# Kernel optimization log

Measured on AMD Instinct MI355X. Metric: run time of the kernel, lower is better.

Reference implementation:

```python
import jax, jax.numpy as jnp
import numpy as np

HEAD_SIZE = 64
HEADS = 12

def _rope(x):
    # x: [B, L, d]; bert4torch interleaved RoPE: q*cos + rotate_every_two(q)*sin
    L, d = x.shape[-2], x.shape[-1]
    inv_freq = 1.0 / (10000.0 ** (jnp.arange(0, d, 2, dtype=jnp.float32) / d))
    ang = jnp.arange(L, dtype=jnp.float32)[:, None] * inv_freq  # [L, d/2]
    sin = jnp.repeat(jnp.sin(ang), 2, axis=-1)  # [L, d]
    cos = jnp.repeat(jnp.cos(ang), 2, axis=-1)  # [L, d]
    x2 = jnp.stack([-x[..., 1::2], x[..., ::2]], axis=-1).reshape(x.shape)
    return x * cos + x2 * sin

def setup_inputs() -> dict:
    key = jax.random.key(0)
    ks = jax.random.split(key, 4)
    B, L, H = 2, 2048, 1024
    inputs = jax.random.normal(ks[0], (B, L, H), dtype=jnp.float32)
    mask = jnp.ones((B, L), dtype=jnp.int32)
    Wp = jax.random.normal(ks[1], (H, 2 * HEAD_SIZE), dtype=jnp.float32) * (1.0 / np.sqrt(H))
    bp = jnp.zeros((2 * HEAD_SIZE,), dtype=jnp.float32)
    Wq = jax.random.normal(ks[2], (2 * HEAD_SIZE, 2 * HEADS), dtype=jnp.float32) * (1.0 / np.sqrt(2 * HEAD_SIZE))
    bq = jnp.zeros((2 * HEADS,), dtype=jnp.float32)
    return {"inputs": inputs, "mask": mask, "Wp": Wp, "bp": bp, "Wq": Wq, "bq": bq}

def reference(inputs, mask, Wp, bp, Wq, bq):
    B, L, _ = inputs.shape
    seq_out = inputs @ Wp + bp                          # [B, L, 2*hs]
    qw, kw = seq_out[..., :HEAD_SIZE], seq_out[..., HEAD_SIZE:]
    qw, kw = _rope(qw), _rope(kw)
    scores = jnp.einsum('bmd,bnd->bmn', qw, kw) / jnp.sqrt(jnp.float32(HEAD_SIZE))  # [B, L, L]
    # chunk(heads, -1) + stack(-2) == reshape(B, L, heads, 2); transpose(1,2) -> [B, H, L, 2]
    bias = (seq_out @ Wq + bq).reshape(B, L, HEADS, 2) / 2.0
    bias = jnp.transpose(bias, (0, 2, 1, 3))            # [B, H, L, 2]
    logits = scores[:, None] + bias[..., :1] + jnp.swapaxes(bias[..., 1:], 2, 3)  # [B, H, L, L]
    m = mask.astype(bool)
    neg_inf = jnp.float32(-jnp.inf)
    logits = jnp.where(m[:, None, :, None], logits, neg_inf)
    logits = jnp.where(m[:, None, None, :], logits, neg_inf)
    tril = jnp.tril(jnp.ones((L, L), dtype=logits.dtype), -1)
    logits = logits - tril * jnp.float32(1e12)
    return logits
```

## Files before the change

### kernel.cpp

```cpp
#include <hip/hip_runtime.h>
#include <math.h>

#define LSEQ 2048
#define NB 2
#define HDIM 1024
#define NKV 128
#define MALL (NB*LSEQ)
#define KSPLIT 4

__global__ __launch_bounds__(256) void k1_gemm(const float* __restrict__ A,
                                               const float* __restrict__ Wp,
                                               float* __restrict__ Cp) {
    const int nt    = blockIdx.x & 1;
    const int split = blockIdx.x >> 1;
    const int m0 = blockIdx.y * 64;
    const int n0 = nt * 64;
    __shared__ float As[32][68];
    __shared__ float Bs[32][64];
    const int tid = threadIdx.x;
    const int tm = tid & 15;
    const int tn = tid >> 4;
    float acc[4][4] = {};
    for (int kc = 0; kc < 8; ++kc) {
        const int k0 = split*256 + kc*32;
        #pragma unroll
        for (int p = 0; p < 2; ++p) {
            int idx = tid + 256*p;
            int row = idx >> 3, kq = idx & 7;
            float4 a = *(const float4*)(A + (size_t)(m0+row)*HDIM + k0 + 4*kq);
            As[4*kq+0][row] = a.x;
            As[4*kq+1][row] = a.y;
            As[4*kq+2][row] = a.z;
            As[4*kq+3][row] = a.w;
        }
        #pragma unroll
        for (int p = 0; p < 2; ++p) {
            int idx = tid + 256*p;
            int r = idx >> 4, c = idx & 15;
            *(float4*)(&Bs[r][4*c]) = *(const float4*)(Wp + (size_t)(k0+r)*NKV + n0 + 4*c);
        }
        __syncthreads();
        #pragma unroll
        for (int kk = 0; kk < 32; ++kk) {
            float4 av = *(const float4*)(&As[kk][4*tm]);
            float4 bv = *(const float4*)(&Bs[kk][4*tn]);
            float aa[4] = {av.x, av.y, av.z, av.w};
            float bb[4] = {bv.x, bv.y, bv.z, bv.w};
            #pragma unroll
            for (int i = 0; i < 4; ++i)
                #pragma unroll
                for (int j = 0; j < 4; ++j)
                    acc[i][j] = fmaf(aa[i], bb[j], acc[i][j]);
        }
        __syncthreads();
    }
    float* outp = Cp + (size_t)split*MALL*NKV;
    #pragma unroll
    for (int i = 0; i < 4; ++i) {
        float4 v = make_float4(acc[i][0], acc[i][1], acc[i][2], acc[i][3]);
        *(float4*)(outp + (size_t)(m0 + 4*tm + i)*NKV + n0 + 4*tn) = v;
    }
}

__global__ __launch_bounds__(64) void k2_rope_bias(const float* __restrict__ Cp,
        const float* __restrict__ bp, const float* __restrict__ Wq,
        const float* __restrict__ bq, float* __restrict__ qwout,
        float* __restrict__ kwout, float* __restrict__ biasQ,
        float* __restrict__ biasK) {
    const int row = blockIdx.x;
    const int b = row >> 11;
    const int l = row & (LSEQ - 1);
    const int t = threadIdx.x;
    float x0 = bp[2*t], x1 = bp[2*t+1];
    #pragma unroll
    for (int s = 0; s < KSPLIT; ++s) {
        const float* r = Cp + (size_t)s*MALL*NKV + (size_t)row*NKV;
        x0 += r[2*t];
        x1 += r[2*t+1];
    }
    const int p = t & 31;
    float inv = exp2f(-0.41524101186098287f * (float)p);
    float ang = (float)l * inv;
    float sn = sinf(ang), cs = cosf(ang);
    float y0 = x0*cs - x1*sn;
    float y1 = x1*cs + x0*sn;
    float* dst = (t < 32) ? (qwout + (size_t)row*64) : (kwout + (size_t)row*64);
    dst[2*p]   = y0;
    dst[2*p+1] = y1;
    float res = 0.f;
    for (int j = 0; j < 24; ++j) {
        float part = fmaf(x0, Wq[(2*t)*24 + j], x1 * Wq[(2*t+1)*24 + j]);
        #pragma unroll
        for (int off = 32; off > 0; off >>= 1)
            part += __shfl_xor(part, off);
        if (t == j) res = part;
    }
    if (t < 24) {
        float v = (res + bq[t]) * 0.5f;
        int h = t >> 1;
        float* bb = (t & 1) ? biasK : biasQ;
        bb[((size_t)b*12 + h)*LSEQ + l] = v;
    }
}

__global__ __launch_bounds__(256, 2) void k3_scores(const float* __restrict__ qw,
        const float* __restrict__ kwv, const float* __restrict__ biasQ,
        const float* __restrict__ biasK, const int* __restrict__ mask,
        float* __restrict__ out) {
    const int m0 = blockIdx.x * 4;
    const int b  = blockIdx.y;
    const int tid = threadIdx.x;
    const int nl = tid & 127;
    const int g  = tid >> 7;
    __shared__ float kws[128 * 68];

    const size_t rowbase = (size_t)b * LSEQ;
    const int mA = m0 + 2*g, mB = mA + 1;

    float4 q0[16], q1[16];
    {
        const float4* qp0 = (const float4*)(qw + (rowbase + mA)*64);
        const float4* qp1 = (const float4*)(qw + (rowbase + mB)*64);
        #pragma unroll
        for (int j = 0; j < 16; ++j) { q0[j] = qp0[j]; q1[j] = qp1[j]; }
    }
    float bq0[12], bq1[12];
    #pragma unroll
    for (int h = 0; h < 12; ++h) {
        const float* bqp = biasQ + ((size_t)b*12 + h)*LSEQ;
        bq0[h] = bqp[mA];
        bq1[h] = bqp[mB];
    }
    const bool okmA = mask[rowbase + mA] != 0;
    const bool okmB = mask[rowbase + mB] != 0;
    const size_t outbase = (size_t)b * 12 * LSEQ * LSEQ;

    for (int c = 0; c < 16; ++c) {
        const int nbase = c * 128;
        __syncthreads();
        #pragma unroll
        for (int p = 0; p < 8; ++p) {
            int f4 = tid + 256*p;
            int r = f4 >> 4, q16 = f4 & 15;
            float4 v = *(const float4*)(kwv + (rowbase + nbase + r)*64 + 4*q16);
            *(float4*)(&kws[r*68 + 4*q16]) = v;
        }
        __syncthreads();

        const int n = nbase + nl;
        float acc0 = 0.f, acc1 = 0.f;
        const float4* kr = (const float4*)(&kws[nl * 68]);
        #pragma unroll
        for (int j = 0; j < 16; ++j) {
            float4 kv = kr[j];
            acc0 = fmaf(q0[j].x, kv.x, acc0);
            acc0 = fmaf(q0[j].y, kv.y, acc0);
            acc0 = fmaf(q0[j].z, kv.z, acc0);
            acc0 = fmaf(q0[j].w, kv.w, acc0);
            acc1 = fmaf(q1[j].x, kv.x, acc1);
            acc1 = fmaf(q1[j].y, kv.y, acc1);
            acc1 = fmaf(q1[j].z, kv.z, acc1);
            acc1 = fmaf(q1[j].w, kv.w, acc1);
        }
        acc0 *= 0.125f;
        acc1 *= 0.125f;

        const bool okn = mask[rowbase + n] != 0;
        const float penA = (mA > n) ? 1e12f : 0.f;
        const float penB = (mB > n) ? 1e12f : 0.f;
        const bool okA = okmA && okn;
        const bool okB = okmB && okn;
        size_t offA = outbase + (size_t)mA * LSEQ + n;
        const float* bkp = biasK + (size_t)b*12*LSEQ + n;
        #pragma unroll
        for (int h = 0; h < 12; ++h) {
            float bk = bkp[(size_t)h * LSEQ];
            float v0 = acc0 + bq0[h] + bk;
            v0 = okA ? v0 : -INFINITY;
            v0 -= penA;
            float v1 = acc1 + bq1[h] + bk;
            v1 = okB ? v1 : -INFINITY;
            v1 -= penB;
            __builtin_nontemporal_store(v0, &out[offA + (size_t)h*LSEQ*LSEQ]);
            __builtin_nontemporal_store(v1, &out[offA + LSEQ + (size_t)h*LSEQ*LSEQ]);
        }
    }
}

extern "C" void kernel_launch(void* const* d_in, const int* in_sizes, int n_in,
                              void* d_out, int out_size, void* d_ws, size_t ws_size,
                              hipStream_t stream) {
    const float* inputs = (const float*)d_in[0];
    const int*   mask   = (const int*)  d_in[1];
    const float* Wp     = (const float*)d_in[2];
    const float* bp     = (const float*)d_in[3];
    const float* Wq     = (const float*)d_in[4];
    const float* bq     = (const float*)d_in[5];
    float* out = (float*)d_out;

    float* Cp  = (float*)d_ws;
    float* qwb = Cp  + (size_t)KSPLIT*MALL*NKV;
    float* kwb = qwb + (size_t)MALL*64;
    float* bQ  = kwb + (size_t)MALL*64;
    float* bK  = bQ  + (size_t)NB*12*LSEQ;

    k1_gemm     <<<dim3(8, 64),   256, 0, stream>>>(inputs, Wp, Cp);
    k2_rope_bias<<<dim3(MALL),     64, 0, stream>>>(Cp, bp, Wq, bq, qwb, kwb, bQ, bK);
    k3_scores   <<<dim3(512, 2), 256, 0, stream>>>(qwb, kwb, bQ, bK, mask, out);
}
```

Measured before the change: 465.9 us.

## Vectorize score stores, widen K tiles with swizzled LDS, retile projection GEMM

Measured after the change: 894.8 us. +92.1%, slower.

```diff
diff --git a/kernel.cpp b/kernel.cpp
--- a/kernel.cpp
+++ b/kernel.cpp
@@ -6,23 +6,23 @@
 #define HDIM 1024
 #define NKV 128
 #define MALL (NB*LSEQ)
-#define KSPLIT 4
+#define KSPLIT 8
+
+typedef float v4f __attribute__((ext_vector_type(4)));
 
 __global__ __launch_bounds__(256) void k1_gemm(const float* __restrict__ A,
                                                const float* __restrict__ Wp,
                                                float* __restrict__ Cp) {
-    const int nt    = blockIdx.x & 1;
-    const int split = blockIdx.x >> 1;
+    const int split = blockIdx.x;
     const int m0 = blockIdx.y * 64;
-    const int n0 = nt * 64;
     __shared__ float As[32][68];
-    __shared__ float Bs[32][64];
+    __shared__ float Bs[32][128];
     const int tid = threadIdx.x;
     const int tm = tid & 15;
     const int tn = tid >> 4;
-    float acc[4][4] = {};
-    for (int kc = 0; kc < 8; ++kc) {
-        const int k0 = split*256 + kc*32;
+    float acc[4][8] = {};
+    for (int kc = 0; kc < 4; ++kc) {
+        const int k0 = split*128 + kc*32;
         #pragma unroll
         for (int p = 0; p < 2; ++p) {
             int idx = tid + 256*p;
@@ -34,22 +34,23 @@
             As[4*kq+3][row] = a.w;
         }
         #pragma unroll
-        for (int p = 0; p < 2; ++p) {
+        for (int p = 0; p < 4; ++p) {
             int idx = tid + 256*p;
-            int r = idx >> 4, c = idx & 15;
-            *(float4*)(&Bs[r][4*c]) = *(const float4*)(Wp + (size_t)(k0+r)*NKV + n0 + 4*c);
+            int r = idx >> 5, c = idx & 31;
+            *(float4*)(&Bs[r][4*c]) = *(const float4*)(Wp + (size_t)(k0+r)*NKV + 4*c);
         }
         __syncthreads();
         #pragma unroll
         for (int kk = 0; kk < 32; ++kk) {
-            float4 av = *(const float4*)(&As[kk][4*tm]);
-            float4 bv = *(const float4*)(&Bs[kk][4*tn]);
+            float4 av  = *(const float4*)(&As[kk][4*tm]);
+            float4 bv0 = *(const float4*)(&Bs[kk][8*tn]);
+            float4 bv1 = *(const float4*)(&Bs[kk][8*tn+4]);
             float aa[4] = {av.x, av.y, av.z, av.w};
-            float bb[4] = {bv.x, bv.y, bv.z, bv.w};
+            float bb[8] = {bv0.x, bv0.y, bv0.z, bv0.w, bv1.x, bv1.y, bv1.z, bv1.w};
             #pragma unroll
             for (int i = 0; i < 4; ++i)
                 #pragma unroll
-                for (int j = 0; j < 4; ++j)
+                for (int j = 0; j < 8; ++j)
                     acc[i][j] = fmaf(aa[i], bb[j], acc[i][j]);
         }
         __syncthreads();
@@ -57,8 +58,9 @@
     float* outp = Cp + (size_t)split*MALL*NKV;
     #pragma unroll
     for (int i = 0; i < 4; ++i) {
-        float4 v = make_float4(acc[i][0], acc[i][1], acc[i][2], acc[i][3]);
-        *(float4*)(outp + (size_t)(m0 + 4*tm + i)*NKV + n0 + 4*tn) = v;
+        float* rp = outp + (size_t)(m0 + 4*tm + i)*NKV + 8*tn;
+        *(float4*)(rp)     = make_float4(acc[i][0], acc[i][1], acc[i][2], acc[i][3]);
+        *(float4*)(rp + 4) = make_float4(acc[i][4], acc[i][5], acc[i][6], acc[i][7]);
     }
 }
 
@@ -74,9 +76,9 @@
     float x0 = bp[2*t], x1 = bp[2*t+1];
     #pragma unroll
     for (int s = 0; s < KSPLIT; ++s) {
-        const float* r = Cp + (size_t)s*MALL*NKV + (size_t)row*NKV;
-        x0 += r[2*t];
-        x1 += r[2*t+1];
+        const float2 v = *(const float2*)(Cp + ((size_t)s*MALL + row)*NKV + 2*t);
+        x0 += v.x;
+        x1 += v.y;
     }
     const int p = t & 31;
     float inv = exp2f(-0.41524101186098287f * (float)p);
@@ -107,15 +109,15 @@
         const float* __restrict__ kwv, const float* __restrict__ biasQ,
         const float* __restrict__ biasK, const int* __restrict__ mask,
         float* __restrict__ out) {
-    const int m0 = blockIdx.x * 4;
+    const int m0 = blockIdx.x * 8;
     const int b  = blockIdx.y;
     const int tid = threadIdx.x;
-    const int nl = tid & 127;
-    const int g  = tid >> 7;
-    __shared__ float kws[128 * 68];
+    const int l   = tid & 63;
+    const int w   = tid >> 6;
+    __shared__ float4 kws4[4096];
 
     const size_t rowbase = (size_t)b * LSEQ;
-    const int mA = m0 + 2*g, mB = mA + 1;
+    const int mA = m0 + 2*w, mB = mA + 1;
 
     float4 q0[16], q1[16];
     {
@@ -134,55 +136,76 @@
     const bool okmA = mask[rowbase + mA] != 0;
     const bool okmB = mask[rowbase + mB] != 0;
     const size_t outbase = (size_t)b * 12 * LSEQ * LSEQ;
-
-    for (int c = 0; c < 16; ++c) {
-        const int nbase = c * 128;
-        __syncthreads();
-        #pragma unroll
-        for (int p = 0; p < 8; ++p) {
-            int f4 = tid + 256*p;
-            int r = f4 >> 4, q16 = f4 & 15;
-            float4 v = *(const float4*)(kwv + (rowbase + nbase + r)*64 + 4*q16);
-            *(float4*)(&kws[r*68 + 4*q16]) = v;
-        }
-        __syncthreads();
-
-        const int n = nbase + nl;
-        float acc0 = 0.f, acc1 = 0.f;
-        const float4* kr = (const float4*)(&kws[nl * 68]);
+    const float4* kg = (const float4*)(kwv + rowbase*64);
+
+    for (int c = 0; c < 8; ++c) {
+        const int nb = c * 256;
+        __syncthreads();
+        #pragma unroll 4
+        for (int p = 0; p < 16; ++p) {
+            int f4id = tid + 256*p;
+            int r = f4id >> 4, q = f4id & 15;
+            float4 v = kg[(size_t)(nb + r)*16 + q];
+            kws4[r*16 + ((q + (r >> 2)) & 15)] = v;
+        }
+        __syncthreads();
+
+        float accA[4] = {}, accB[4] = {};
         #pragma unroll
         for (int j = 0; j < 16; ++j) {
-            float4 kv = kr[j];
-            acc0 = fmaf(q0[j].x, kv.x, acc0);
-            acc0 = fmaf(q0[j].y, kv.y, acc0);
-            acc0 = fmaf(q0[j].z, kv.z, acc0);
-            acc0 = fmaf(q0[j].w, kv.w, acc0);
-            acc1 = fmaf(q1[j].x, kv.x, acc1);
-            acc1 = fmaf(q1[j].y, kv.y, acc1);
-            acc1 = fmaf(q1[j].z, kv.z, acc1);
-            acc1 = fmaf(q1[j].w, kv.w, acc1);
-        }
-        acc0 *= 0.125f;
-        acc1 *= 0.125f;
-
-        const bool okn = mask[rowbase + n] != 0;
-        const float penA = (mA > n) ? 1e12f : 0.f;
-        const float penB = (mB > n) ? 1e12f : 0.f;
-        const bool okA = okmA && okn;
-        const bool okB = okmB && okn;
-        size_t offA = outbase + (size_t)mA * LSEQ + n;
-        const float* bkp = biasK + (size_t)b*12*LSEQ + n;
+            const int rot = (j + l) & 15;
+            float4 k0v = kws4[(4*l + 0)*16 + rot];
+            float4 k1v = kws4[(4*l + 1)*16 + rot];
+            float4 k2v = kws4[(4*l + 2)*16 + rot];
+            float4 k3v = kws4[(4*l + 3)*16 + rot];
+            float4 qa = q0[j], qb = q1[j];
+            accA[0] = fmaf(qa.x, k0v.x, accA[0]); accA[0] = fmaf(qa.y, k0v.y, accA[0]);
+            accA[0] = fmaf(qa.z, k0v.z, accA[0]); accA[0] = fmaf(qa.w, k0v.w, accA[0]);
+            accA[1] = fmaf(qa.x, k1v.x, accA[1]); accA[1] = fmaf(qa.y, k1v.y, accA[1]);
+            accA[1] = fmaf(qa.z, k1v.z, accA[1]); accA[1] = fmaf(qa.w, k1v.w, accA[1]);
+            accA[2] = fmaf(qa.x, k2v.x, accA[2]); accA[2] = fmaf(qa.y, k2v.y, accA[2]);
+            accA[2] = fmaf(qa.z, k2v.z, accA[2]); accA[2] = fmaf(qa.w, k2v.w, accA[2]);
+            accA[3] = fmaf(qa.x, k3v.x, accA[3]); accA[3] = fmaf(qa.y, k3v.y, accA[3]);
+            accA[3] = fmaf(qa.z, k3v.z, accA[3]); accA[3] = fmaf(qa.w, k3v.w, accA[3]);
+            accB[0] = fmaf(qb.x, k0v.x, accB[0]); accB[0] = fmaf(qb.y, k0v.y, accB[0]);
+            accB[0] = fmaf(qb.z, k0v.z, accB[0]); accB[0] = fmaf(qb.w, k0v.w, accB[0]);
+            accB[1] = fmaf(qb.x, k1v.x, accB[1]); accB[1] = fmaf(qb.y, k1v.y, accB[1]);
+            accB[1] = fmaf(qb.z, k1v.z, accB[1]); accB[1] = fmaf(qb.w, k1v.w, accB[1]);
+            accB[2] = fmaf(qb.x, k2v.x, accB[2]); accB[2] = fmaf(qb.y, k2v.y, accB[2]);
+            accB[2] = fmaf(qb.z, k2v.z, accB[2]); accB[2] = fmaf(qb.w, k2v.w, accB[2]);
+            accB[3] = fmaf(qb.x, k3v.x, accB[3]); accB[3] = fmaf(qb.y, k3v.y, accB[3]);
+            accB[3] = fmaf(qb.z, k3v.z, accB[3]); accB[3] = fmaf(qb.w, k3v.w, accB[3]);
+        }
+
+        const int n0 = nb + 4*l;
+        const int4 mv = *(const int4*)(mask + rowbase + n0);
+        const int okn[4] = {mv.x != 0, mv.y != 0, mv.z != 0, mv.w != 0};
+        float baseA[4], baseB[4];
+        #pragma unroll
+        for (int i = 0; i < 4; ++i) {
+            const int n = n0 + i;
+            baseA[i] = (okmA && okn[i]) ? (accA[i]*0.125f - ((mA > n) ? 1e12f : 0.f))
+                                        : -INFINITY;
+            baseB[i] = (okmB && okn[i]) ? (accB[i]*0.125f - ((mB > n) ? 1e12f : 0.f))
+                                        : -INFINITY;
+        }
+        const float* bkbase = biasK + (size_t)b*12*LSEQ + n0;
+        float* outA = out + outbase + (size_t)mA*LSEQ + n0;
         #pragma unroll
         for (int h = 0; h < 12; ++h) {
-            float bk = bkp[(size_t)h * LSEQ];
-            float v0 = acc0 + bq0[h] + bk;
-            v0 = okA ? v0 : -INFINITY;
-            v0 -= penA;
-            float v1 = acc1 + bq1[h] + bk;
-            v1 = okB ? v1 : -INFINITY;
-            v1 -= penB;
-            __builtin_nontemporal_store(v0, &out[offA + (size_t)h*LSEQ*LSEQ]);
-            __builtin_nontemporal_store(v1, &out[offA + LSEQ + (size_t)h*LSEQ*LSEQ]);
+            float4 bk = *(const float4*)(bkbase + (size_t)h*LSEQ);
+            v4f vA, vB;
+            vA.x = baseA[0] + bq0[h] + bk.x;
+            vA.y = baseA[1] + bq0[h] + bk.y;
+            vA.z = baseA[2] + bq0[h] + bk.z;
+            vA.w = baseA[3] + bq0[h] + bk.w;
+            vB.x = baseB[0] + bq1[h] + bk.x;
+            vB.y = baseB[1] + bq1[h] + bk.y;
+            vB.z = baseB[2] + bq1[h] + bk.z;
+            vB.w = baseB[3] + bq1[h] + bk.w;
+            float* po = outA + (size_t)h*LSEQ*LSEQ;
+            __builtin_nontemporal_store(vA, (v4f*)po);
+            __builtin_nontemporal_store(vB, (v4f*)(po + LSEQ));
         }
     }
 }
@@ -204,7 +227,7 @@
     float* bQ  = kwb + (size_t)MALL*64;
     float* bK  = bQ  + (size_t)NB*12*LSEQ;
 
-    k1_gemm     <<<dim3(8, 64),   256, 0, stream>>>(inputs, Wp, Cp);
-    k2_rope_bias<<<dim3(MALL),     64, 0, stream>>>(Cp, bp, Wq, bq, qwb, kwb, bQ, bK);
-    k3_scores   <<<dim3(512, 2), 256, 0, stream>>>(qwb, kwb, bQ, bK, mask, out);
-}
+    k1_gemm     <<<dim3(KSPLIT, 64), 256, 0, stream>>>(inputs, Wp, Cp);
+    k2_rope_bias<<<dim3(MALL),        64, 0, stream>>>(Cp, bp, Wq, bq, qwb, kwb, bQ, bK);
+    k3_scores   <<<dim3(256, 2),     256, 0, stream>>>(qwb, kwb, bQ, bK, mask, out);
+}
```
